# Performance work log

Hardware: AMD Instinct MI355X
Metric: run time of the kernel (lower is better)

The kernel has to match this reference:

```python
import jax, jax.numpy as jnp
import numpy as np

B, T, D = 4, 4000, 1024
H = 8
DK = D // H          # key dim per head; value dim per head also DK (value_factor=1)
CHUNK = 500
EPS_LN = 1e-5
EPS_RMS = 1e-6


def rotate_every_two(x):
    x1 = x[..., ::2]
    x2 = x[..., 1::2]
    return jnp.stack((-x2, x1), axis=-1).reshape(x.shape)


def theta_shift(x, sin, cos):
    # x: [b,h,t,dk]; sin/cos: [t,dk]
    return x * cos + rotate_every_two(x) * sin


def rel_pos(slen, chunk_len, num_heads, key_dim):
    # RetNetRelPos(chunkwise_recurrent=True)
    angle = 1.0 / (10000 ** jnp.linspace(0.0, 1.0, key_dim // 2))
    angle = jnp.repeat(angle, 2)  # == unsqueeze(-1).repeat(1,2).flatten()
    decay = jnp.log(1.0 - 2.0 ** (-5.0 - jnp.arange(num_heads, dtype=jnp.float32)))
    index = jnp.arange(slen, dtype=jnp.float32)
    sin = jnp.sin(index[:, None] * angle[None, :])  # [t,dk]
    cos = jnp.cos(index[:, None] * angle[None, :])
    bi = jnp.arange(chunk_len, dtype=jnp.float32)
    tril = jnp.tril(jnp.ones((chunk_len, chunk_len), bool))
    diff = bi[:, None] - bi[None, :]
    mask = jnp.where(tril[None], jnp.exp(decay[:, None, None] * diff[None]), 0.0)  # [H,C,C]
    last_row = mask[:, -1]                                            # [H,C]
    value_inner_decay = (last_row / last_row.sum(-1, keepdims=True))[:, :, None]  # [H,C,1]
    scale = jnp.sqrt(mask.sum(-1, keepdims=True))                     # [H,C,1]
    inner_mask = mask / scale
    cross_decay = jnp.exp(decay * chunk_len)[:, None, None]           # [H,1,1]
    qid = jnp.exp(decay[:, None] * (bi + 1.0))[:, :, None]            # [H,C,1]
    query_inner_decay = qid / (scale / last_row.sum(-1)[:, None, None])
    return (sin, cos), (inner_mask, cross_decay, query_inner_decay, value_inner_decay)


def retention_chunkwise(qr, kr, v, inner):
    mask, cross_decay, query_inner_decay, value_inner_decay = inner
    b, t = v.shape[0], v.shape[1]
    C = mask.shape[1]
    n = t // C
    h, dk = qr.shape[1], qr.shape[3]
    dv = v.shape[2] // h
    # [b,h,t,dk] -> [b,n,h,C,dk]
    qr = qr.transpose(0, 2, 1, 3).reshape(b, n, C, h, dk).transpose(0, 1, 3, 2, 4)
    kr = kr.transpose(0, 2, 1, 3).reshape(b, n, C, h, dk).transpose(0, 1, 3, 2, 4)
    v = v.reshape(b, n, C, h, dv).transpose(0, 1, 3, 2, 4)  # [b,n,h,C,dv]

    qk = jnp.einsum('bnhcd,bnhed->bnhce', qr, kr) * mask  # [b,n,h,C,C]
    inner_scale = jnp.clip(jnp.abs(jax.lax.stop_gradient(qk)).sum(-1, keepdims=True), 1.0, None)
    qk = qk / inner_scale
    inner_output = jnp.einsum('bnhce,bnhed->bnhcd', qk, v)  # [b,n,h,C,dv]

    kv = jnp.einsum('bnhck,bnhcv->bnhkv', kr, v * value_inner_decay)  # [b,n,h,dk,dv]

    def step(carry, kv_i):
        kv_state, kv_scale = carry
        out = (kv_state / kv_scale, kv_scale)
        new_state = kv_state * cross_decay + kv_i
        sg = jnp.abs(jax.lax.stop_gradient(new_state)).sum(-2, keepdims=True).max(-1, keepdims=True)
        return (new_state, jnp.clip(sg, 1.0, None)), out

    init = (jnp.zeros((b, h, dk, dv), v.dtype), jnp.ones((b, h, 1, 1), v.dtype))
    _, (kv_rec, cross_scale) = jax.lax.scan(step, init, jnp.moveaxis(kv, 1, 0))
    kv_rec = jnp.moveaxis(kv_rec, 0, 1)            # [b,n,h,dk,dv]
    cross_scale = jnp.moveaxis(cross_scale, 0, 1)  # [b,n,h,1,1]

    all_scale = jnp.maximum(inner_scale, cross_scale)
    cross_output = jnp.einsum('bnhcd,bnhdv->bnhcv', qr * query_inner_decay, kv_rec)
    output = inner_output / (all_scale / inner_scale) + cross_output / (all_scale / cross_scale)
    return output.transpose(0, 1, 3, 2, 4).reshape(b, t, h, dv)  # [b,t,h,dv]


def setup_inputs() -> dict:
    key = jax.random.key(0)
    ks = jax.random.split(key, 6)
    s = 0.02
    return {
        'inputs': jax.random.normal(ks[0], (B, T, D), jnp.float32),
        'ln_gamma': jnp.ones((D,), jnp.float32),
        'ln_beta': jnp.zeros((D,), jnp.float32),
        'Wq': jax.random.normal(ks[1], (D, D), jnp.float32) * s,
        'Wk': jax.random.normal(ks[2], (D, D), jnp.float32) * s,
        'Wv': jax.random.normal(ks[3], (D, D), jnp.float32) * s,
        'Wg': jax.random.normal(ks[4], (D, D), jnp.float32) * s,
        'Wo': jax.random.normal(ks[5], (D, D), jnp.float32) * s,
    }


def reference(inputs, ln_gamma, ln_beta, Wq, Wk, Wv, Wg, Wo):
    b, t, d = inputs.shape
    # pre-LayerNorm
    mu = inputs.mean(-1, keepdims=True)
    var = ((inputs - mu) ** 2).mean(-1, keepdims=True)
    x = (inputs - mu) / jnp.sqrt(var + EPS_LN) * ln_gamma + ln_beta

    (sin, cos), inner = rel_pos(t, CHUNK, H, DK)

    q = (x @ Wq).reshape(b, t, H, DK).transpose(0, 2, 1, 3)
    k = (x @ Wk * (DK ** -0.5)).reshape(b, t, H, DK).transpose(0, 2, 1, 3)
    v = x @ Wv
    g = x @ Wg

    qr = theta_shift(q, sin, cos)
    kr = theta_shift(k, sin, cos)

    out = retention_chunkwise(qr, kr, v, inner)  # [b,t,H,dv]
    # group norm: per-head RMSNorm without affine
    out = out * jax.lax.rsqrt(jnp.mean(out ** 2, -1, keepdims=True) + EPS_RMS)
    out = out.reshape(b, t, H * DK)
    out = jax.nn.silu(g) * out
    return out @ Wo  # dropout is identity in eval
```

## Files before the change

kernel.cpp:

```cpp
#include <hip/hip_runtime.h>
#include <hip/hip_bf16.h>


typedef __attribute__((ext_vector_type(4))) float f32x4;
typedef __attribute__((ext_vector_type(8))) short s16x8;

#define DEV static __device__ __forceinline__

DEV float bfu(ushort u){ union{uint i; float f;} x; x.i=((uint)u)<<16; return x.f; }
DEV float bflo(uint w){ union{uint i; float f;} x; x.i=w<<16; return x.f; }
DEV float bfhi(uint w){ union{uint i; float f;} x; x.i=w&0xffff0000u; return x.f; }
DEV ushort f2bf(float f){ union{float f; uint u;} x; x.f=f; uint r = x.u + 0x7fffu + ((x.u>>16)&1u); return (ushort)(r>>16); }
DEV uint pack2(float lo, float hi){ return ((uint)f2bf(hi)<<16) | (uint)f2bf(lo); }

DEV void gload16(const ushort* g, ushort* l) {
  __builtin_amdgcn_global_load_lds((const __attribute__((address_space(1))) void*)g,
                                   (__attribute__((address_space(3))) void*)l, 16, 0, 0);
}

__global__ __launch_bounds__(256) void f2bf_t_all(const float* __restrict__ s0, const float* __restrict__ s1,
                                                  const float* __restrict__ s2, const float* __restrict__ s3,
                                                  const float* __restrict__ s4,
                                                  ushort* __restrict__ d0, ushort* __restrict__ d1,
                                                  ushort* __restrict__ d2, ushort* __restrict__ d3,
                                                  ushort* __restrict__ d4) {
  const float* src; ushort* dst;
  switch (blockIdx.z) {
    case 0: src=s0; dst=d0; break;
    case 1: src=s1; dst=d1; break;
    case 2: src=s2; dst=d2; break;
    case 3: src=s3; dst=d3; break;
    default: src=s4; dst=d4; break;
  }
  __shared__ ushort t[64][72];
  int kt = blockIdx.x*64, nt = blockIdx.y*64;
  int tid = threadIdx.x;
  int r = tid>>2, c0 = (tid&3)*16;
  const float* s = src + (size_t)(kt+r)*1024 + nt + c0;
  #pragma unroll
  for (int j=0;j<16;j+=4) {
    float4 vv = *(const float4*)(s+j);
    t[r][c0+j]=f2bf(vv.x); t[r][c0+j+1]=f2bf(vv.y); t[r][c0+j+2]=f2bf(vv.z); t[r][c0+j+3]=f2bf(vv.w);
  }
  __syncthreads();
  union { uint4 u4[2]; ushort s16[16]; } tmp;
  #pragma unroll
  for (int j=0;j<16;j++) tmp.s16[j] = t[c0+j][r];
  ushort* d = dst + (size_t)(nt+r)*1024 + kt + c0;
  *(uint4*)(d)   = tmp.u4[0];
  *(uint4*)(d+8) = tmp.u4[1];
}

__global__ __launch_bounds__(256) void ln_kernel(const float* __restrict__ x,
                                                 const float* __restrict__ gamma,
                                                 const float* __restrict__ beta,
                                                 ushort* __restrict__ xo) {
  int row = blockIdx.x;
  int tid = threadIdx.x;
  const float* xr = x + (size_t)row*1024;
  float4 u = ((const float4*)xr)[tid];
  float s = u.x+u.y+u.z+u.w;
  float sq = u.x*u.x+u.y*u.y+u.z*u.z+u.w*u.w;
  #pragma unroll
  for (int o=32;o;o>>=1){ s += __shfl_xor(s,o); sq += __shfl_xor(sq,o); }
  __shared__ float red[8];
  int wv=tid>>6, ln=tid&63;
  if (ln==0){ red[wv]=s; red[4+wv]=sq; }
  __syncthreads();
  s = red[0]+red[1]+red[2]+red[3];
  sq = red[4]+red[5]+red[6]+red[7];
  float mu = s*(1.0f/1024.0f);
  float var = sq*(1.0f/1024.0f)-mu*mu;
  float inv = rsqrtf(var+1e-5f);
  float4 gg = ((const float4*)gamma)[tid];
  float4 bb = ((const float4*)beta)[tid];
  float o0=(u.x-mu)*inv*gg.x+bb.x;
  float o1=(u.y-mu)*inv*gg.y+bb.y;
  float o2=(u.z-mu)*inv*gg.z+bb.z;
  float o3=(u.w-mu)*inv*gg.w+bb.w;
  uint2 w; w.x=pack2(o0,o1); w.y=pack2(o2,o3);
  ((uint2*)(xo+(size_t)row*1024))[tid]=w;
}

__global__ __launch_bounds__(256) void sincos_kernel(uint* __restrict__ cstab) {
  int idx = blockIdx.x*256+threadIdx.x;
  if (idx >= 4000*64) return;
  int t = idx>>6, i = idx&63;
  float ang = expf(-9.210340371976184f * (float)i * (1.0f/63.0f));
  float a = (float)t * ang;
  float sv = sinf(a), cv = cosf(a);
  uint p = pack2(cv, sv);
  cstab[(size_t)t*128+2*i]   = p;
  cstab[(size_t)t*128+2*i+1] = p;
}

__global__ __launch_bounds__(256) void gemm_proj(const ushort* __restrict__ A,
                                                 const ushort* __restrict__ BT,
                                                 ushort* __restrict__ qb,
                                                 ushort* __restrict__ kb,
                                                 ushort* __restrict__ gb,
                                                 ushort* __restrict__ kT,
                                                 ushort* __restrict__ vT,
                                                 const uint* __restrict__ cstab) {
  __attribute__((aligned(16))) __shared__ char smem[34816];
  ushort* As = (ushort*)smem;
  ushort* Bs = (ushort*)(smem+16384);
  const int K = 1024;
  int wg = blockIdx.x;
  int s, r9, sm;
  if (wg < 3584) { s = wg>>9; r9 = wg&511; sm = 16; }
  else           { s = 7;     r9 = wg-3584; sm = 13; }
  int nblk = r9 / sm;
  int mloc = r9 - nblk*sm;
  int bm = (s*16 + mloc)*128, bn = nblk*128;
  int tid = threadIdx.x;
  int w = tid>>6, l = tid&63;
  int wm = (w>>1)*64, wn = (w&1)*64;
  int rsel = l&15, ko = (l>>4)*8;
  f32x4 acc[4][4];
  #pragma unroll
  for (int a2=0;a2<4;a2++)
    #pragma unroll
    for (int j=0;j<4;j++){ acc[a2][j][0]=0; acc[a2][j][1]=0; acc[a2][j][2]=0; acc[a2][j][3]=0; }
  const ushort* ap0 = A  + (size_t)(bm + w*32 + (l>>2))*K + (l&3)*8;
  const ushort* ap1 = ap0 + (size_t)16*K;
  const ushort* bp0 = BT + (size_t)(bn + w*32 + (l>>2))*K + (l&3)*8;
  const ushort* bp1 = bp0 + (size_t)16*K;
  {
    ushort* ab = As + w*1024; ushort* bb2 = Bs + w*1024;
    gload16(ap0, ab); gload16(ap1, ab+512);
    gload16(bp0, bb2); gload16(bp1, bb2+512);
  }
  int cur = 0;
  for (int kt=0; kt<K; kt+=32) {
    __syncthreads();
    if (kt+32 < K) {
      int nb = cur^1;
      ushort* ab = As + nb*4096 + w*1024; ushort* bb2 = Bs + nb*4096 + w*1024;
      gload16(ap0+kt+32, ab); gload16(ap1+kt+32, ab+512);
      gload16(bp0+kt+32, bb2); gload16(bp1+kt+32, bb2+512);
    }
    const ushort* Ac = As + cur*4096;
    const ushort* Bc = Bs + cur*4096;
    s16x8 af[4], bfr[4];
    #pragma unroll
    for (int mf=0;mf<4;mf++) af[mf]  = *(const s16x8*)&Ac[(wm+mf*16+rsel)*32 + ko];
    #pragma unroll
    for (int nf=0;nf<4;nf++) bfr[nf] = *(const s16x8*)&Bc[(wn+nf*16+rsel)*32 + ko];
    #pragma unroll
    for (int mf=0;mf<4;mf++)
      #pragma unroll
      for (int nf=0;nf<4;nf++)
        acc[mf][nf] = __builtin_amdgcn_mfma_f32_16x16x32_bf16(af[mf], bfr[nf], acc[mf][nf], 0,0,0);
    cur ^= 1;
  }
  int proj = bn>>10;
  int bnp  = bn&1023;
  int hh   = bnp>>7;
  __syncthreads();
  ushort* Ct = (ushort*)smem;
  if (proj < 2) {
    float decay = logf(1.0f - exp2f(-5.0f-(float)hh));
    float ksc = 0.08838834764831845f;
    #pragma unroll
    for (int mf=0;mf<4;mf++) {
      #pragma unroll
      for (int r2=0;r2<4;r2++) {
        int rowt = wm+mf*16+(l>>4)*4+r2;
        int grow = bm+rowt;
        int t = grow - (grow/4000)*4000;
        int cch = t - (t/500)*500;
        float esc = (proj==0)? expf(decay*(float)cch) : expf(-decay*(float)cch)*ksc;
        const uint* cst = cstab + (size_t)t*128;
        #pragma unroll
        for (int nf=0;nf<4;nf++) {
          int colt = wn+nf*16+(l&15);
          float vv = acc[mf][nf][r2];
          uint wcs = cst[colt];
          float cc = bflo(wcs), ss = bfhi(wcs);
          float ov = __shfl_xor(vv,1);
          float rot = ((l&1)==0)? (vv*cc-ov*ss) : (vv*cc+ov*ss);
          Ct[rowt*136+colt] = f2bf(rot*esc);
        }
      }
    }
  } else {
    #pragma unroll
    for (int mf=0;mf<4;mf++)
      #pragma unroll
      for (int nf=0;nf<4;nf++) {
        int colt = wn+nf*16+(l&15);
        #pragma unroll
        for (int r2=0;r2<4;r2++)
          Ct[(wm+mf*16+(l>>4)*4+r2)*136+colt] = f2bf(acc[mf][nf][r2]);
      }
  }
  __syncthreads();
  if (proj != 2) {
    ushort* dst = (proj==0)? qb : (proj==1)? kb : gb;
    int r = tid>>1, ch=(tid&1)*64;
    ushort* drow = dst + (size_t)(bm+r)*1024 + bnp + ch;
    #pragma unroll
    for (int j=0;j<8;j++) *(uint4*)(drow+j*8) = *(uint4*)&Ct[r*136+ch+j*8];
  }
  if (proj==1 || proj==2) {
    ushort* Tdst = (proj==1)? kT : vT;
    int dloc = tid>>1, rh=(tid&1)*64;
    #pragma unroll
    for (int j=0;j<8;j++) {
      int gr = bm + rh + j*8;
      int bb = gr/4000; int t0 = gr - bb*4000;
      int ch0 = t0/500; int c0 = t0 - ch0*500;
      if (c0 <= 492) {
        union{uint4 u; ushort s[8];} pk;
        #pragma unroll
        for (int ii=0;ii<8;ii++) pk.s[ii] = Ct[(rh+j*8+ii)*136 + dloc];
        *(uint4*)(Tdst + ((size_t)(bb*64+ch0*8+hh))*65536 + (size_t)dloc*512 + c0) = pk.u;
      } else {
        #pragma unroll
        for (int ii=0;ii<8;ii++) {
          int gri = gr+ii; int bbi=gri/4000; int ti=gri-bbi*4000; int chi=ti/500; int ci=ti-chi*500;
          Tdst[((size_t)(bbi*64+chi*8+hh))*65536 + (size_t)dloc*512 + ci] = Ct[(rh+j*8+ii)*136+dloc];
        }
      }
    }
  }
}

__global__ __launch_bounds__(256) void gemm_out(const ushort* __restrict__ A,
                                                const ushort* __restrict__ BT,
                                                float* __restrict__ C) {
  __attribute__((aligned(16))) __shared__ char smem[34816];
  ushort* As = (ushort*)smem;
  ushort* Bs = (ushort*)(smem+16384);
  const int K = 1024;
  int wg = blockIdx.x;
  int s, r9, sm;
  if (wg < 896) { s = wg>>7; r9 = wg&127; sm = 16; }
  else          { s = 7;     r9 = wg-896; sm = 13; }
  int nblk = r9 / sm;
  int mloc = r9 - nblk*sm;
  int bm = (s*16 + mloc)*128, bn = nblk*128;
  int tid = threadIdx.x;
  int w = tid>>6, l = tid&63;
  int wm = (w>>1)*64, wn = (w&1)*64;
  int rsel = l&15, ko = (l>>4)*8;
  f32x4 acc[4][4];
  #pragma unroll
  for (int a2=0;a2<4;a2++)
    #pragma unroll
    for (int j=0;j<4;j++){ acc[a2][j][0]=0; acc[a2][j][1]=0; acc[a2][j][2]=0; acc[a2][j][3]=0; }
  const ushort* ap0 = A  + (size_t)(bm + w*32 + (l>>2))*K + (l&3)*8;
  const ushort* ap1 = ap0 + (size_t)16*K;
  const ushort* bp0 = BT + (size_t)(bn + w*32 + (l>>2))*K + (l&3)*8;
  const ushort* bp1 = bp0 + (size_t)16*K;
  {
    ushort* ab = As + w*1024; ushort* bb2 = Bs + w*1024;
    gload16(ap0, ab); gload16(ap1, ab+512);
    gload16(bp0, bb2); gload16(bp1, bb2+512);
  }
  int cur = 0;
  for (int kt=0; kt<K; kt+=32) {
    __syncthreads();
    if (kt+32 < K) {
      int nb = cur^1;
      ushort* ab = As + nb*4096 + w*1024; ushort* bb2 = Bs + nb*4096 + w*1024;
      gload16(ap0+kt+32, ab); gload16(ap1+kt+32, ab+512);
      gload16(bp0+kt+32, bb2); gload16(bp1+kt+32, bb2+512);
    }
    const ushort* Ac = As + cur*4096;
    const ushort* Bc = Bs + cur*4096;
    s16x8 af[4], bfr[4];
    #pragma unroll
    for (int mf=0;mf<4;mf++) af[mf]  = *(const s16x8*)&Ac[(wm+mf*16+rsel)*32 + ko];
    #pragma unroll
    for (int nf=0;nf<4;nf++) bfr[nf] = *(const s16x8*)&Bc[(wn+nf*16+rsel)*32 + ko];
    #pragma unroll
    for (int mf=0;mf<4;mf++)
      #pragma unroll
      for (int nf=0;nf<4;nf++)
        acc[mf][nf] = __builtin_amdgcn_mfma_f32_16x16x32_bf16(af[mf], bfr[nf], acc[mf][nf], 0,0,0);
    cur ^= 1;
  }
  __syncthreads();
  float* Cf = (float*)smem;
  #pragma unroll
  for (int half=0; half<2; half++) {
    if ((w>>1)==half) {
      #pragma unroll
      for (int mf=0;mf<4;mf++)
        #pragma unroll
        for (int nf=0;nf<4;nf++)
          #pragma unroll
          for (int r2=0;r2<4;r2++)
            Cf[(mf*16+(l>>4)*4+r2)*132 + wn+nf*16+(l&15)] = acc[mf][nf][r2];
    }
    __syncthreads();
    {
      int r = tid>>2, cs=(tid&3)*32;
      float* drow = C + (size_t)(bm+half*64+r)*1024 + bn + cs;
      #pragma unroll
      for (int j=0;j<8;j++) *(float4*)(drow+j*4) = *(float4*)&Cf[r*132+cs+j*4];
    }
    __syncthreads();
  }
}

__global__ __launch_bounds__(256) void kv_mfma(const ushort* __restrict__ kT,
                                               const ushort* __restrict__ vT,
                                               float* __restrict__ kvp) {
  int bnh = blockIdx.x;
  __shared__ ushort sh2[16384];
  int tid=threadIdx.x;
  int wv=tid>>6, l=tid&63, g=l>>4, c16=l&15;
  int wr = wv>>1, wc = wv&1;
  int ri[4], ro[4];
  #pragma unroll
  for (int jj=0;jj<4;jj++){
    int i = wv*256 + jj*64 + l;
    ri[jj] = i>>3;
    ro[jj] = (((i&7)*16) ^ ((ri[jj]&7)<<4))>>1;
  }
  const ushort* kbase = kT + (size_t)bnh*65536;
  const ushort* vbase = vT + (size_t)bnh*65536;
  f32x4 acc[4][4];
  #pragma unroll
  for (int i=0;i<4;i++)
    #pragma unroll
    for (int j=0;j<4;j++){ acc[i][j][0]=0; acc[i][j][1]=0; acc[i][j][2]=0; acc[i][j][3]=0; }
  for (int ctep=0; ctep<8; ctep++) {
    int cb = ctep*64;
    __syncthreads();
    #pragma unroll
    for (int jj=0;jj<4;jj++){
      gload16(kbase + (size_t)ri[jj]*512 + cb + ro[jj], (ushort*)((char*)sh2 + wv*4096 + jj*1024));
      gload16(vbase + (size_t)ri[jj]*512 + cb + ro[jj], (ushort*)((char*)sh2 + 16384 + wv*4096 + jj*1024));
    }
    __syncthreads();
    if (ctep==7) {
      for (int z=tid; z<128*12; z+=256) {
        int r = z/12, j = 52 + (z - (z/12)*12);
        *(ushort*)((char*)sh2 + 16384 + r*128 + ((j*2) ^ ((r&7)<<4))) = 0;
      }
      __syncthreads();
    }
    #pragma unroll
    for (int kc=0;kc<2;kc++) {
      s16x8 af[4], bf2[4];
      #pragma unroll
      for (int mf=0;mf<4;mf++){
        int row = wr*64+mf*16+c16;
        af[mf] = *(const s16x8*)((const char*)sh2 + row*128 + ((((kc*32+g*8)*2)) ^ ((row&7)<<4)));
      }
      #pragma unroll
      for (int nf=0;nf<4;nf++){
        int row = wc*64+nf*16+c16;
        bf2[nf] = *(const s16x8*)((const char*)sh2 + 16384 + row*128 + ((((kc*32+g*8)*2)) ^ ((row&7)<<4)));
      }
      #pragma unroll
      for (int mf=0;mf<4;mf++)
        #pragma unroll
        for (int nf=0;nf<4;nf++)
          acc[mf][nf] = __builtin_amdgcn_mfma_f32_16x16x32_bf16(af[mf], bf2[nf], acc[mf][nf], 0,0,0);
    }
  }
  float* outp = kvp + (size_t)bnh*16384;
  #pragma unroll
  for (int mf=0;mf<4;mf++)
    #pragma unroll
    for (int nf=0;nf<4;nf++)
      #pragma unroll
      for (int reg=0;reg<4;reg++)
        outp[(size_t)(wr*64+mf*16+g*4+reg)*128 + wc*64+nf*16+c16] = acc[mf][nf][reg];
}

__global__ __launch_bounds__(256) void scan_kernel(const float* __restrict__ kvp,
                                                   ushort* __restrict__ kvrecT,
                                                   float* __restrict__ crosssc) {
  int bh = blockIdx.x;
  int b = bh>>3, h = bh&7;
  float Dh = 1.0f - exp2f(-5.0f-(float)h);
  float decay = logf(Dh);
  float cd = expf(decay*500.0f);
  float ls = (1.0f - expf(decay*500.0f))/(1.0f-Dh);
  float cst = expf(decay*499.0f)/ls;
  int tid=threadIdx.x;
  int vcol = tid&127, khalf = tid>>7;
  float st[64];
  #pragma unroll
  for (int i=0;i<64;i++) st[i]=0;
  float scale = 1.0f;
  __shared__ float colpart[2][128];
  __shared__ float sred[2];
  for (int n=0;n<8;n++) {
    int bnh = (b*8+n)*8+h;
    const float* src = kvp + (size_t)bnh*16384;
    ushort* rec = kvrecT + (size_t)bnh*16384;
    float inv = 1.0f/scale;
    float cs = 0;
    #pragma unroll
    for (int i=0;i<64;i++) {
      int kk = khalf*64+i;
      rec[(size_t)vcol*128+kk] = f2bf(st[i]*inv);
      st[i] = st[i]*cd + cst*src[(size_t)kk*128+vcol];
      cs += fabsf(st[i]);
    }
    if (tid==0) crosssc[bnh] = scale;
    colpart[khalf][vcol] = cs;
    __syncthreads();
    if (tid<128) colpart[0][tid] += colpart[1][tid];
    __syncthreads();
    float m = (tid<128)? colpart[0][tid] : 0.0f;
    #pragma unroll
    for (int o=32;o;o>>=1) m = fmaxf(m,__shfl_xor(m,o));
    if (tid<128 && (tid&63)==0) sred[tid>>6]=m;
    __syncthreads();
    scale = fmaxf(fmaxf(sred[0],sred[1]),1.0f);
    __syncthreads();
  }
}

__global__ __launch_bounds__(256,4) void iout_mfma(const ushort* __restrict__ qr,
                                                   const ushort* __restrict__ kr,
                                                   const ushort* __restrict__ vT,
                                                   const ushort* __restrict__ kvrecT,
                                                   const float* __restrict__ crosssc,
                                                   const ushort* __restrict__ gbuf,
                                                   ushort* __restrict__ opre) {
  int ib = blockIdx.x;
  int x = ib&7, u = ib>>3;
  int rt = u&7;
  int bnh = x*32 + (u>>3);
  int h = bnh&7, n=(bnh>>3)&7, b=bnh>>6;
  size_t base = (size_t)(b*4000+n*500)*1024 + h*128;
  float Dh = 1.0f - exp2f(-5.0f-(float)h);
  float decay = logf(Dh);
  __shared__ ushort sh[20480];
  char* shb = (char*)sh;
  int tid = threadIdx.x;
  int wv = tid>>6, l = tid&63;
  int g = l>>4, c16 = l&15;
  int r_base = rt*64 + wv*16 + g*4;

  int qrow = rt*64 + wv*16 + c16; if (qrow>499) qrow=499;
  s16x8 aq[4];
  #pragma unroll
  for (int kc=0;kc<4;kc++)
    aq[kc] = *(const s16x8*)(qr + base + (size_t)qrow*1024 + kc*32 + g*8);

  int ktrow[4], ktofs[4], vtrow[4], vtofs[4];
  #pragma unroll
  for (int jj=0;jj<4;jj++){
    int i = wv*256 + jj*64 + l;
    int r_ = i>>4;  ktrow[jj]=r_;  ktofs[jj] = (((i&15)*16) ^ ((r_&7)<<4))>>1;
    int r2_ = i>>3; vtrow[jj]=r2_; vtofs[jj] = (((i&7)*16) ^ ((r2_&7)<<4))>>1;
  }
  const ushort* vTb = vT + (size_t)bnh*65536;

  f32x4 pv[8], cc[8];
  #pragma unroll
  for (int i=0;i<8;i++){
    #pragma unroll
    for (int j=0;j<4;j++){ pv[i][j]=0.0f; cc[i][j]=0.0f; }
  }
  float rowsum[4] = {0,0,0,0};

  for (int et=0; et<=rt; et++) {
    __syncthreads();
    #pragma unroll
    for (int jj=0;jj<4;jj++){
      int gr = et*64 + ktrow[jj]; if (gr>499) gr=499;
      gload16(kr + base + (size_t)gr*1024 + ktofs[jj], (ushort*)(shb + wv*4096 + jj*1024));
      gload16(vTb + (size_t)vtrow[jj]*512 + et*64 + vtofs[jj], (ushort*)(shb + 16384 + wv*4096 + jj*1024));
    }
    __syncthreads();
    f32x4 S[4];
    #pragma unroll
    for (int i=0;i<4;i++){ S[i][0]=0; S[i][1]=0; S[i][2]=0; S[i][3]=0; }
    __builtin_amdgcn_s_setprio(1);
    #pragma unroll
    for (int kc=0;kc<4;kc++) {
      #pragma unroll
      for (int ni=0;ni<4;ni++) {
        int krow = ni*16+c16;
        s16x8 bf = *(const s16x8*)(shb + krow*256 + ((((kc*32+g*8)*2)) ^ ((krow&7)<<4)));
        S[ni] = __builtin_amdgcn_mfma_f32_16x16x32_bf16(aq[kc], bf, S[ni], 0,0,0);
      }
    }
    __builtin_amdgcn_s_setprio(0);
    bool diag = (et==rt);
    #pragma unroll
    for (int ni=0;ni<4;ni++) {
      int e_rel = et*64 + ni*16 + c16;
      #pragma unroll
      for (int reg=0;reg<4;reg++) {
        float p = S[ni][reg];
        if (diag && e_rel > r_base+reg) p = 0.0f;
        rowsum[reg] += fabsf(p);
        int prow = wv*16 + g*4 + reg;
        *(ushort*)(shb + 32768 + prow*128 + (((ni*16+c16)*2) ^ ((prow&7)<<4))) = f2bf(p);
      }
    }
    __builtin_amdgcn_s_setprio(1);
    #pragma unroll
    for (int kc=0;kc<2;kc++) {
      int prow = wv*16 + c16;
      s16x8 pa = *(const s16x8*)(shb + 32768 + prow*128 + ((((kc*32+g*8)*2)) ^ ((prow&7)<<4)));
      #pragma unroll
      for (int nf=0;nf<8;nf++) {
        int vrow = nf*16+c16;
        s16x8 vb = *(const s16x8*)(shb + 16384 + vrow*128 + ((((kc*32+g*8)*2)) ^ ((vrow&7)<<4)));
        pv[nf] = __builtin_amdgcn_mfma_f32_16x16x32_bf16(pa, vb, pv[nf], 0,0,0);
      }
    }
    __builtin_amdgcn_s_setprio(0);
  }
  #pragma unroll
  for (int reg=0;reg<4;reg++) {
    float s = rowsum[reg];
    s += __shfl_xor(s,1); s += __shfl_xor(s,2); s += __shfl_xor(s,4); s += __shfl_xor(s,8);
    rowsum[reg] = s;
  }
  __syncthreads();
  #pragma unroll
  for (int jj=0;jj<8;jj++){
    int i = wv*512 + jj*64 + l;
    int r_ = i>>4;
    int ofs = (((i&15)*16) ^ ((r_&7)<<4))>>1;
    gload16(kvrecT + (size_t)bnh*16384 + (size_t)r_*128 + ofs, (ushort*)(shb + wv*8192 + jj*1024));
  }
  __syncthreads();
  __builtin_amdgcn_s_setprio(1);
  #pragma unroll
  for (int kc=0;kc<4;kc++) {
    #pragma unroll
    for (int nf=0;nf<8;nf++) {
      int krow = nf*16+c16;
      s16x8 bb = *(const s16x8*)(shb + krow*256 + ((((kc*32+g*8)*2)) ^ ((krow&7)<<4)));
      cc[nf] = __builtin_amdgcn_mfma_f32_16x16x32_bf16(aq[kc], bb, cc[nf], 0,0,0);
    }
  }
  __builtin_amdgcn_s_setprio(0);
  float cs = crosssc[bnh];
  float lsum = (1.0f-expf(decay*500.0f))/(1.0f-Dh);
  float ed = expf(decay);
  #pragma unroll
  for (int reg=0;reg<4;reg++) {
    int rr = r_base + reg;
    if (rr < 500) {
      float rs = (1.0f-expf(decay*(float)(rr+1)))/(1.0f-Dh);
      float rsr = rsqrtf(rs);
      float is = fmaxf(1.0f, rowsum[reg]*rsr);
      float all = fmaxf(is, cs);
      float qid = ed*lsum*rsr;
      float fi = rsr/all;
      float fc = qid*(cs/all);
      float o[8]; float ssq = 0.0f;
      #pragma unroll
      for (int nf=0;nf<8;nf++){ o[nf] = pv[nf][reg]*fi + cc[nf][reg]*fc; ssq += o[nf]*o[nf]; }
      ssq += __shfl_xor(ssq,1); ssq += __shfl_xor(ssq,2); ssq += __shfl_xor(ssq,4); ssq += __shfl_xor(ssq,8);
      float rmss = rsqrtf(ssq*(1.0f/128.0f)+1e-6f);
      size_t rowoff = (size_t)(b*4000+n*500+rr)*1024 + h*128;
      #pragma unroll
      for (int nf=0;nf<8;nf++){
        float gv = bfu(gbuf[rowoff + nf*16 + c16]);
        float sg = gv/(1.0f+expf(-gv));
        opre[rowoff + nf*16 + c16] = f2bf(sg*o[nf]*rmss);
      }
    }
  }
}

extern "C" void kernel_launch(void* const* d_in, const int* in_sizes, int n_in,
                              void* d_out, int out_size, void* d_ws, size_t ws_size,
                              hipStream_t stream) {
  const float* x     = (const float*)d_in[0];
  const float* gamma = (const float*)d_in[1];
  const float* beta  = (const float*)d_in[2];
  const float* Wq    = (const float*)d_in[3];
  const float* Wk    = (const float*)d_in[4];
  const float* Wv    = (const float*)d_in[5];
  const float* Wg    = (const float*)d_in[6];
  const float* Wo    = (const float*)d_in[7];
  float* out = (float*)d_out;

  char* ws = (char*)d_ws;
  size_t off = 0;
  auto alloc = [&](size_t bytes)->void* { void* p = ws+off; off += (bytes+255)&~(size_t)255; return p; };
  const size_t BT1024 = (size_t)16000*1024;
  ushort* xln  = (ushort*)alloc(BT1024*2);
  ushort* q    = (ushort*)alloc(BT1024*2);
  ushort* k    = (ushort*)alloc(BT1024*2);
  ushort* g    = (ushort*)alloc(BT1024*2);
  ushort* WqT  = (ushort*)alloc((size_t)1024*1024*2);
  ushort* WkT  = (ushort*)alloc((size_t)1024*1024*2);
  ushort* WvT  = (ushort*)alloc((size_t)1024*1024*2);
  ushort* WgT  = (ushort*)alloc((size_t)1024*1024*2);
  ushort* WoT  = (ushort*)alloc((size_t)1024*1024*2);
  uint* cstab  = (uint*)alloc((size_t)4000*128*4);
  ushort* kT   = (ushort*)alloc((size_t)256*65536*2);
  ushort* vT   = (ushort*)alloc((size_t)256*65536*2);
  ushort* kvrecT=(ushort*)alloc((size_t)256*16384*2);
  float* crosssc = (float*)alloc(256*4);
  (void)ws_size; (void)in_sizes; (void)n_in; (void)out_size;

  ln_kernel<<<16000,256,0,stream>>>(x,gamma,beta,xln);
  sincos_kernel<<<1000,256,0,stream>>>(cstab);
  dim3 tt(16,16,5);
  f2bf_t_all<<<tt,256,0,stream>>>(Wq,Wk,Wv,Wg,Wo, WqT,WkT,WvT,WgT,WoT);

  gemm_proj<<<4000,256,0,stream>>>(xln, WqT, q, k, g, kT, vT, cstab);

  float* kvp = (float*)xln;
  kv_mfma<<<256,256,0,stream>>>(kT,vT,kvp);
  scan_kernel<<<32,256,0,stream>>>(kvp,kvrecT,crosssc);

  ushort* opre = xln;
  iout_mfma<<<2048,256,0,stream>>>(q,k,vT,kvrecT,crosssc,g,opre);

  gemm_out<<<1000,256,0,stream>>>(opre,WoT,out);
}
```

Before: 392.8 us.

## Triple-buffer GEMM LDS pipeline with vmcnt waits and widen scan kernel

```diff
diff --git a/kernel.cpp b/kernel.cpp
--- a/kernel.cpp
+++ b/kernel.cpp
@@ -102,9 +102,7 @@
                                                  ushort* __restrict__ kT,
                                                  ushort* __restrict__ vT,
                                                  const uint* __restrict__ cstab) {
-  __attribute__((aligned(16))) __shared__ char smem[34816];
-  ushort* As = (ushort*)smem;
-  ushort* Bs = (ushort*)(smem+16384);
+  __attribute__((aligned(16))) __shared__ char smem[49152];
   const int K = 1024;
   int wg = blockIdx.x;
   int s, r9, sm;
@@ -127,21 +125,29 @@
   const ushort* bp0 = BT + (size_t)(bn + w*32 + (l>>2))*K + (l&3)*8;
   const ushort* bp1 = bp0 + (size_t)16*K;
   {
-    ushort* ab = As + w*1024; ushort* bb2 = Bs + w*1024;
-    gload16(ap0, ab); gload16(ap1, ab+512);
-    gload16(bp0, bb2); gload16(bp1, bb2+512);
+    char* buf = smem;
+    gload16(ap0, (ushort*)(buf + w*2048));
+    gload16(ap1, (ushort*)(buf + w*2048 + 1024));
+    gload16(bp0, (ushort*)(buf + 8192 + w*2048));
+    gload16(bp1, (ushort*)(buf + 8192 + w*2048 + 1024));
   }
   int cur = 0;
-  for (int kt=0; kt<K; kt+=32) {
-    __syncthreads();
-    if (kt+32 < K) {
-      int nb = cur^1;
-      ushort* ab = As + nb*4096 + w*1024; ushort* bb2 = Bs + nb*4096 + w*1024;
-      gload16(ap0+kt+32, ab); gload16(ap1+kt+32, ab+512);
-      gload16(bp0+kt+32, bb2); gload16(bp1+kt+32, bb2+512);
-    }
-    const ushort* Ac = As + cur*4096;
-    const ushort* Bc = Bs + cur*4096;
+  for (int it=0; it<32; ++it) {
+    if (it+1 < 32) {
+      int nb = cur+1; if (nb==3) nb=0;
+      char* buf = smem + nb*16384;
+      int kt = (it+1)*32;
+      gload16(ap0+kt, (ushort*)(buf + w*2048));
+      gload16(ap1+kt, (ushort*)(buf + w*2048 + 1024));
+      gload16(bp0+kt, (ushort*)(buf + 8192 + w*2048));
+      gload16(bp1+kt, (ushort*)(buf + 8192 + w*2048 + 1024));
+      asm volatile("s_waitcnt vmcnt(4)" ::: "memory");
+    } else {
+      asm volatile("s_waitcnt vmcnt(0)" ::: "memory");
+    }
+    __builtin_amdgcn_s_barrier();
+    const ushort* Ac = (const ushort*)(smem + cur*16384);
+    const ushort* Bc = (const ushort*)(smem + cur*16384 + 8192);
     s16x8 af[4], bfr[4];
     #pragma unroll
     for (int mf=0;mf<4;mf++) af[mf]  = *(const s16x8*)&Ac[(wm+mf*16+rsel)*32 + ko];
@@ -152,7 +158,7 @@
       #pragma unroll
       for (int nf=0;nf<4;nf++)
         acc[mf][nf] = __builtin_amdgcn_mfma_f32_16x16x32_bf16(af[mf], bfr[nf], acc[mf][nf], 0,0,0);
-    cur ^= 1;
+    cur = (cur+1==3)? 0 : cur+1;
   }
   int proj = bn>>10;
   int bnp  = bn&1023;
@@ -230,9 +236,7 @@
 __global__ __launch_bounds__(256) void gemm_out(const ushort* __restrict__ A,
                                                 const ushort* __restrict__ BT,
                                                 float* __restrict__ C) {
-  __attribute__((aligned(16))) __shared__ char smem[34816];
-  ushort* As = (ushort*)smem;
-  ushort* Bs = (ushort*)(smem+16384);
+  __attribute__((aligned(16))) __shared__ char smem[49152];
   const int K = 1024;
   int wg = blockIdx.x;
   int s, r9, sm;
@@ -255,21 +259,29 @@
   const ushort* bp0 = BT + (size_t)(bn + w*32 + (l>>2))*K + (l&3)*8;
   const ushort* bp1 = bp0 + (size_t)16*K;
   {
-    ushort* ab = As + w*1024; ushort* bb2 = Bs + w*1024;
-    gload16(ap0, ab); gload16(ap1, ab+512);
-    gload16(bp0, bb2); gload16(bp1, bb2+512);
+    char* buf = smem;
+    gload16(ap0, (ushort*)(buf + w*2048));
+    gload16(ap1, (ushort*)(buf + w*2048 + 1024));
+    gload16(bp0, (ushort*)(buf + 8192 + w*2048));
+    gload16(bp1, (ushort*)(buf + 8192 + w*2048 + 1024));
   }
   int cur = 0;
-  for (int kt=0; kt<K; kt+=32) {
-    __syncthreads();
-    if (kt+32 < K) {
-      int nb = cur^1;
-      ushort* ab = As + nb*4096 + w*1024; ushort* bb2 = Bs + nb*4096 + w*1024;
-      gload16(ap0+kt+32, ab); gload16(ap1+kt+32, ab+512);
-      gload16(bp0+kt+32, bb2); gload16(bp1+kt+32, bb2+512);
-    }
-    const ushort* Ac = As + cur*4096;
-    const ushort* Bc = Bs + cur*4096;
+  for (int it=0; it<32; ++it) {
+    if (it+1 < 32) {
+      int nb = cur+1; if (nb==3) nb=0;
+      char* buf = smem + nb*16384;
+      int kt = (it+1)*32;
+      gload16(ap0+kt, (ushort*)(buf + w*2048));
+      gload16(ap1+kt, (ushort*)(buf + w*2048 + 1024));
+      gload16(bp0+kt, (ushort*)(buf + 8192 + w*2048));
+      gload16(bp1+kt, (ushort*)(buf + 8192 + w*2048 + 1024));
+      asm volatile("s_waitcnt vmcnt(4)" ::: "memory");
+    } else {
+      asm volatile("s_waitcnt vmcnt(0)" ::: "memory");
+    }
+    __builtin_amdgcn_s_barrier();
+    const ushort* Ac = (const ushort*)(smem + cur*16384);
+    const ushort* Bc = (const ushort*)(smem + cur*16384 + 8192);
     s16x8 af[4], bfr[4];
     #pragma unroll
     for (int mf=0;mf<4;mf++) af[mf]  = *(const s16x8*)&Ac[(wm+mf*16+rsel)*32 + ko];
@@ -280,7 +292,7 @@
       #pragma unroll
       for (int nf=0;nf<4;nf++)
         acc[mf][nf] = __builtin_amdgcn_mfma_f32_16x16x32_bf16(af[mf], bfr[nf], acc[mf][nf], 0,0,0);
-    cur ^= 1;
+    cur = (cur+1==3)? 0 : cur+1;
   }
   __syncthreads();
   float* Cf = (float*)smem;
@@ -374,7 +386,7 @@
         outp[(size_t)(wr*64+mf*16+g*4+reg)*128 + wc*64+nf*16+c16] = acc[mf][nf][reg];
 }
 
-__global__ __launch_bounds__(256) void scan_kernel(const float* __restrict__ kvp,
+__global__ __launch_bounds__(512) void scan_kernel(const float* __restrict__ kvp,
                                                    ushort* __restrict__ kvrecT,
                                                    float* __restrict__ crosssc) {
   int bh = blockIdx.x;
@@ -385,12 +397,12 @@
   float ls = (1.0f - expf(decay*500.0f))/(1.0f-Dh);
   float cst = expf(decay*499.0f)/ls;
   int tid=threadIdx.x;
-  int vcol = tid&127, khalf = tid>>7;
-  float st[64];
-  #pragma unroll
-  for (int i=0;i<64;i++) st[i]=0;
+  int vcol = tid&127, kq = tid>>7;
+  float st[32];
+  #pragma unroll
+  for (int i=0;i<32;i++) st[i]=0;
   float scale = 1.0f;
-  __shared__ float colpart[2][128];
+  __shared__ float colpart[4][128];
   __shared__ float sred[2];
   for (int n=0;n<8;n++) {
     int bnh = (b*8+n)*8+h;
@@ -399,16 +411,16 @@
     float inv = 1.0f/scale;
     float cs = 0;
     #pragma unroll
-    for (int i=0;i<64;i++) {
-      int kk = khalf*64+i;
+    for (int i=0;i<32;i++) {
+      int kk = kq*32+i;
       rec[(size_t)vcol*128+kk] = f2bf(st[i]*inv);
       st[i] = st[i]*cd + cst*src[(size_t)kk*128+vcol];
       cs += fabsf(st[i]);
     }
     if (tid==0) crosssc[bnh] = scale;
-    colpart[khalf][vcol] = cs;
-    __syncthreads();
-    if (tid<128) colpart[0][tid] += colpart[1][tid];
+    colpart[kq][vcol] = cs;
+    __syncthreads();
+    if (tid<128) colpart[0][tid] += colpart[1][tid] + colpart[2][tid] + colpart[3][tid];
     __syncthreads();
     float m = (tid<128)? colpart[0][tid] : 0.0f;
     #pragma unroll
@@ -613,7 +625,7 @@
 
   float* kvp = (float*)xln;
   kv_mfma<<<256,256,0,stream>>>(kT,vT,kvp);
-  scan_kernel<<<32,256,0,stream>>>(kvp,kvrecT,crosssc);
+  scan_kernel<<<32,512,0,stream>>>(kvp,kvrecT,crosssc);
 
   ushort* opre = xln;
   iout_mfma<<<2048,256,0,stream>>>(q,k,vT,kvrecT,crosssc,g,opre);
```

Result: slower. 423.5 us (+7.8%).
